# Kernel tuning notes

Measured on AMD Instinct MI355X. Metric: run time of the kernel, lower is better.

## Reference

```python
import jax, jax.numpy as jnp
import numpy as np

D = 1024          # d_model / hidden_size
F = 2048          # d_ff / intermediate_size
E = 7             # routed experts = num_experts(8) - num_shared(1)
K = 2             # top_k
AUX_COEF = 0.01


def setup_inputs() -> dict:
    key = jax.random.key(0)
    ks = jax.random.split(key, 6)
    std = 0.02
    x = jax.random.normal(ks[0], (2, 1024, D), dtype=jnp.float32)
    router_w = jax.random.normal(ks[1], (E, D), dtype=jnp.float32) * std      # Linear(D->E), no bias
    cfc_w = jax.random.normal(ks[2], (E, 2 * F, D), dtype=jnp.float32) * std  # fused gate+up per expert
    cproj_w = jax.random.normal(ks[3], (E, D, F), dtype=jnp.float32) * std    # down proj per expert
    shared_fc_w = jax.random.normal(ks[4], (2 * F, D), dtype=jnp.float32) * std
    shared_proj_w = jax.random.normal(ks[5], (D, F), dtype=jnp.float32) * std
    return {"x": x, "router_w": router_w, "cfc_w": cfc_w, "cproj_w": cproj_w,
            "shared_fc_w": shared_fc_w, "shared_proj_w": shared_proj_w}


def reference(x, router_w, cfc_w, cproj_w, shared_fc_w, shared_proj_w):
    b, s, d = x.shape
    T = b * s
    xt = x.reshape(T, d)                                     # [T, D]

    # ---- router: softmax + top-k, renormalized gates ----
    logits = xt @ router_w.T                                 # [T, E]
    probs = jax.nn.softmax(logits, axis=-1)                  # [T, E]
    topv, topi = jax.lax.top_k(probs, K)                     # [T, K]
    gates = topv / jnp.sum(topv, axis=-1, keepdims=True)     # [T, K]
    oh = jax.nn.one_hot(topi, E, dtype=probs.dtype)          # [T, K, E]
    combine = jnp.einsum('tk,tke->te', gates, oh)            # [T, E] sparse combine weights

    # ---- grouped-GEMM SwiGLU experts (dense dispatch over E) ----
    h = jnp.einsum('td,efd->tef', xt, cfc_w)                 # [T, E, 2F]
    g, u = jnp.split(h, 2, axis=-1)                          # [T, E, F] each
    act = jax.nn.silu(g) * u                                 # [T, E, F]
    act = act * combine[..., None]                           # weight before down-proj
    y = jnp.einsum('tef,edf->td', act, cproj_w)              # [T, D]

    # ---- load-balancing aux loss ----
    tokens_per_expert = jnp.mean(jnp.sum(oh, axis=1), axis=0) / K  # [E]
    mean_probs = jnp.mean(probs, axis=0)                            # [E]
    aux = (E * jnp.sum(tokens_per_expert * mean_probs)) * AUX_COEF

    # ---- shared expert (single SwiGLU, num_shared_experts == 1) ----
    hs = xt @ shared_fc_w.T                                  # [T, 2F]
    gs, us = jnp.split(hs, 2, axis=-1)
    shared = (jax.nn.silu(gs) * us) @ shared_proj_w.T        # [T, D]

    y = y + shared
    return y.reshape(b, s, d), aux.astype(x.dtype)
```

## Files before the change

### kernel.cpp

```cpp
#include <hip/hip_runtime.h>

#define TT 2048
#define DM 1024
#define FF 2048
#define NE 7
#define NSLOT 6144
#define H_LD 4096

typedef short bf16x8 __attribute__((ext_vector_type(8)));
typedef float f32x4 __attribute__((ext_vector_type(4)));

__device__ __forceinline__ unsigned short f2bf(float f) {
  union { float f; unsigned int u; } v; v.f = f;
  unsigned int r = v.u + 0x7fffu + ((v.u >> 16) & 1u);
  return (unsigned short)(r >> 16);
}
__device__ __forceinline__ float bf2f(unsigned short s) {
  union { unsigned int u; float f; } v; v.u = ((unsigned int)s) << 16;
  return v.f;
}

#define GLDS16(gp, lp)                                                        \
  __builtin_amdgcn_global_load_lds(                                           \
      (const __attribute__((address_space(1))) void*)(gp),                    \
      (__attribute__((address_space(3))) void*)(lp), 16, 0, 0)

__global__ __launch_bounds__(256) void convert_kernel(
    const float* __restrict__ src, unsigned short* __restrict__ dst) {
  size_t i = ((size_t)blockIdx.x * 256 + threadIdx.x) * 8;
  float4 a = *(const float4*)(src + i);
  float4 b = *(const float4*)(src + i + 4);
  bf16x8 o;
  o[0]=(short)f2bf(a.x); o[1]=(short)f2bf(a.y); o[2]=(short)f2bf(a.z); o[3]=(short)f2bf(a.w);
  o[4]=(short)f2bf(b.x); o[5]=(short)f2bf(b.y); o[6]=(short)f2bf(b.z); o[7]=(short)f2bf(b.w);
  *(bf16x8*)(dst + i) = o;
}

__global__ __launch_bounds__(256) void router_kernel(
    const float* __restrict__ x, const float* __restrict__ rw,
    int* __restrict__ cnt, float* __restrict__ probsum,
    int* __restrict__ idxl, float* __restrict__ gwl) {
  __shared__ float ps[NE];
  int tid = threadIdx.x;
  if (tid < NE) ps[tid] = 0.f;
  __syncthreads();
  int wave = tid >> 6, lane = tid & 63;
  int t = blockIdx.x * 4 + wave;
  float xv[16];
#pragma unroll
  for (int i = 0; i < 16; ++i) xv[i] = x[(size_t)t * DM + lane + i * 64];
  float lg[NE];
#pragma unroll
  for (int e = 0; e < NE; ++e) {
    float s = 0.f;
#pragma unroll
    for (int i = 0; i < 16; ++i) s += xv[i] * rw[e * DM + lane + i * 64];
#pragma unroll
    for (int o = 32; o > 0; o >>= 1) s += __shfl_xor(s, o);
    lg[e] = s;
  }
  float m = lg[0];
#pragma unroll
  for (int e = 1; e < NE; ++e) m = fmaxf(m, lg[e]);
  float p[NE]; float sum = 0.f;
#pragma unroll
  for (int e = 0; e < NE; ++e) { p[e] = expf(lg[e] - m); sum += p[e]; }
  float inv = 1.f / sum;
  int i1 = 0; float v1 = p[0];
#pragma unroll
  for (int e = 1; e < NE; ++e) if (p[e] > v1) { v1 = p[e]; i1 = e; }
  int i2 = -1; float v2 = -1.f;
#pragma unroll
  for (int e = 0; e < NE; ++e) if (e != i1 && p[e] > v2) { v2 = p[e]; i2 = e; }
  float g1 = v1 / (v1 + v2), g2 = v2 / (v1 + v2);
  if (lane == 0) {
#pragma unroll
    for (int e = 0; e < NE; ++e) atomicAdd(&ps[e], p[e] * inv);
    int pos = atomicAdd(&cnt[i1], 1); idxl[i1 * TT + pos] = t; gwl[i1 * TT + pos] = g1;
    pos = atomicAdd(&cnt[i2], 1);     idxl[i2 * TT + pos] = t; gwl[i2 * TT + pos] = g2;
    idxl[NE * TT + t] = t; gwl[NE * TT + t] = 1.0f;
  }
  __syncthreads();
  if (tid < NE) atomicAdd(&probsum[tid], ps[tid]);
}

__global__ void finalize_kernel(int* __restrict__ cnt, int* __restrict__ offs,
                                const float* __restrict__ probsum,
                                float* __restrict__ aux_out) {
  if (threadIdx.x == 0) {
    int o = 0;
    for (int e = 0; e < NE; ++e) { offs[e] = o; o += cnt[e]; }
    offs[NE] = o;
    cnt[NE] = TT;
    double s = 0.0;
    for (int e = 0; e < NE; ++e) s += (double)cnt[e] * (double)probsum[e];
    aux_out[0] = (float)(0.01 * 7.0 * s / (4096.0 * 2048.0));
  }
}

__global__ __launch_bounds__(256) void compact_kernel(
    const int* __restrict__ cnt, const int* __restrict__ offs,
    const int* __restrict__ idxl, const float* __restrict__ gwl,
    int* __restrict__ token_s, float* __restrict__ gate_s) {
  int j = blockIdx.x * 256 + threadIdx.x;
  int e = j >> 11, pos = j & 2047;
  if (pos < cnt[e]) {
    int s = offs[e] + pos;
    token_s[s] = idxl[j];
    gate_s[s] = gwl[j];
  }
}

template <int MODE>
__global__ __launch_bounds__(256) void moe_gemm2_kernel(
    const unsigned short* __restrict__ Abase,
    const unsigned short* __restrict__ Wb,
    unsigned short* __restrict__ ActOut, float* __restrict__ Yout,
    const int* __restrict__ cnt, const int* __restrict__ offs,
    const int* __restrict__ token_s, const float* __restrict__ gate_s) {
  constexpr int NB = (MODE == 0) ? 8 : 4;
  constexpr int BROWS = NB * 16;
  constexpr int K = (MODE == 0) ? 1024 : 2048;
  constexpr int LDA = (MODE == 0) ? 1024 : 2048;
  constexpr int WSTRIDE = (MODE == 0) ? 4096 * 1024 : 1024 * 2048;

  __shared__ unsigned short As[128 * 32];
  __shared__ unsigned short Bs[BROWS * 32];

  const int e = blockIdx.z;
  const int cnt_e = cnt[e];
  const int m0 = blockIdx.y * 128;
  if (m0 >= cnt_e) return;
  const int off_e = offs[e];
  const int nb = blockIdx.x;
  const unsigned short* Bw = Wb + (size_t)e * WSTRIDE;

  const int tid = threadIdx.x;
  const int w = tid >> 6, l = tid & 63;
  const int kq = l & 3;
  const int lsub = l >> 2;

  const unsigned short* aSrc0;
  const unsigned short* aSrc1;
  {
    int r0 = w * 32 + lsub, r1 = r0 + 16;
    int rr0 = min(m0 + r0, cnt_e - 1), rr1 = min(m0 + r1, cnt_e - 1);
    int arow0 = (MODE == 0) ? token_s[off_e + rr0] : (off_e + rr0);
    int arow1 = (MODE == 0) ? token_s[off_e + rr1] : (off_e + rr1);
    aSrc0 = Abase + (size_t)arow0 * LDA + kq * 8;
    aSrc1 = Abase + (size_t)arow1 * LDA + kq * 8;
  }
  unsigned short* aDst0 = &As[(w * 32) * 32];
  unsigned short* aDst1 = &As[(w * 32 + 16) * 32];

  const unsigned short* bSrc0;
  const unsigned short* bSrc1 = nullptr;
  unsigned short* bDst0;
  unsigned short* bDst1 = nullptr;
  if (MODE == 0) {
    int r0 = w * 32 + lsub, r1 = r0 + 16;
    int w0 = (r0 < 64) ? nb * 64 + r0 : 2048 + nb * 64 + (r0 - 64);
    int w1 = (r1 < 64) ? nb * 64 + r1 : 2048 + nb * 64 + (r1 - 64);
    bSrc0 = Bw + (size_t)w0 * K + kq * 8;
    bSrc1 = Bw + (size_t)w1 * K + kq * 8;
    bDst0 = &Bs[(w * 32) * 32];
    bDst1 = &Bs[(w * 32 + 16) * 32];
  } else {
    int r0 = w * 16 + lsub;
    bSrc0 = Bw + (size_t)(nb * 64 + r0) * K + kq * 8;
    bDst0 = &Bs[(w * 16) * 32];
  }

  f32x4 acc[2][NB];
#pragma unroll
  for (int m = 0; m < 2; ++m)
#pragma unroll
    for (int n = 0; n < NB; ++n) acc[m][n] = (f32x4){0.f, 0.f, 0.f, 0.f};

  const int lr = l & 15, lh = l >> 4;

  for (int k0 = 0; k0 < K; k0 += 32) {
    __syncthreads();
    GLDS16(aSrc0 + k0, aDst0);
    GLDS16(aSrc1 + k0, aDst1);
    GLDS16(bSrc0 + k0, bDst0);
    if (MODE == 0) GLDS16(bSrc1 + k0, bDst1);
    __syncthreads();
    bf16x8 af[2], bfv[NB];
#pragma unroll
    for (int m = 0; m < 2; ++m)
      af[m] = *(const bf16x8*)&As[(w * 32 + m * 16 + lr) * 32 + lh * 8];
#pragma unroll
    for (int n = 0; n < NB; ++n)
      bfv[n] = *(const bf16x8*)&Bs[(n * 16 + lr) * 32 + lh * 8];
#pragma unroll
    for (int m = 0; m < 2; ++m)
#pragma unroll
      for (int n = 0; n < NB; ++n)
        acc[m][n] = __builtin_amdgcn_mfma_f32_16x16x32_bf16(af[m], bfv[n], acc[m][n], 0, 0, 0);
  }

#pragma unroll
  for (int m = 0; m < 2; ++m) {
#pragma unroll
    for (int j = 0; j < 4; ++j) {
      int r = w * 32 + m * 16 + lh * 4 + j;
      int gm = m0 + r;
      if (gm < cnt_e) {
        if (MODE == 0) {
          float gate = gate_s[off_e + gm];
          size_t base = (size_t)(off_e + gm) * FF + nb * 64;
#pragma unroll
          for (int n = 0; n < 4; ++n) {
            float g = acc[m][n][j], u = acc[m][n + 4][j];
            float sg = g / (1.f + __expf(-g));
            ActOut[base + n * 16 + lr] = f2bf(sg * u * gate);
          }
        } else {
          int tok = token_s[off_e + gm];
          size_t base = (size_t)tok * DM + nb * 64;
#pragma unroll
          for (int n = 0; n < 4; ++n)
            atomicAdd(&Yout[base + n * 16 + lr], acc[m][n][j]);
        }
      }
    }
  }
}

template <int MODE>
__global__ __launch_bounds__(256) void legacy_gemm_kernel(
    const unsigned short* __restrict__ Abase,
    const float* __restrict__ Bw_routed, const float* __restrict__ Bw_shared,
    unsigned short* __restrict__ Hout, float* __restrict__ Yout,
    const int* __restrict__ cnt, const int* __restrict__ offs,
    const int* __restrict__ token_s, int N, int K, int lda) {
  __shared__ unsigned short As[128 * 32];
  __shared__ unsigned short Bs[128 * 32];
  const int e = blockIdx.z;
  const int cnt_e = cnt[e];
  const int m0 = blockIdx.y * 128;
  if (m0 >= cnt_e) return;
  const int off_e = offs[e];
  const int n0 = blockIdx.x * 128;
  const float* Bw = (e == NE) ? Bw_shared : Bw_routed + (size_t)e * N * K;
  const int tid = threadIdx.x;
  const int wave = tid >> 6, lane = tid & 63;
  const int srow = tid >> 1, kh = tid & 1;
  int rr = min(m0 + srow, cnt_e - 1);
  int slot = off_e + rr;
  int arow = (MODE == 0) ? token_s[slot] : slot;
  const unsigned short* ap = Abase + (size_t)arow * lda + kh * 16;
  const float* bp = Bw + (size_t)(n0 + srow) * K + kh * 16;
  unsigned short* adst = &As[srow * 32 + kh * 16];
  unsigned short* bdst = &Bs[srow * 32 + kh * 16];
  f32x4 acc[4][4];
#pragma unroll
  for (int m = 0; m < 4; ++m)
#pragma unroll
    for (int n = 0; n < 4; ++n) acc[m][n] = (f32x4){0.f, 0.f, 0.f, 0.f};
  const int wr = wave >> 1, wc = wave & 1;
  const int lr = lane & 15, lh = lane >> 4;
  for (int k0 = 0; k0 < K; k0 += 32) {
    __syncthreads();
    bf16x8 a0 = *(const bf16x8*)(ap + k0);
    bf16x8 a1 = *(const bf16x8*)(ap + k0 + 8);
    float4 b0 = *(const float4*)(bp + k0);
    float4 b1 = *(const float4*)(bp + k0 + 4);
    float4 b2 = *(const float4*)(bp + k0 + 8);
    float4 b3 = *(const float4*)(bp + k0 + 12);
    *(bf16x8*)adst = a0;
    *(bf16x8*)(adst + 8) = a1;
    bf16x8 w0, w1;
    w0[0]=(short)f2bf(b0.x); w0[1]=(short)f2bf(b0.y); w0[2]=(short)f2bf(b0.z); w0[3]=(short)f2bf(b0.w);
    w0[4]=(short)f2bf(b1.x); w0[5]=(short)f2bf(b1.y); w0[6]=(short)f2bf(b1.z); w0[7]=(short)f2bf(b1.w);
    w1[0]=(short)f2bf(b2.x); w1[1]=(short)f2bf(b2.y); w1[2]=(short)f2bf(b2.z); w1[3]=(short)f2bf(b2.w);
    w1[4]=(short)f2bf(b3.x); w1[5]=(short)f2bf(b3.y); w1[6]=(short)f2bf(b3.z); w1[7]=(short)f2bf(b3.w);
    *(bf16x8*)bdst = w0;
    *(bf16x8*)(bdst + 8) = w1;
    __syncthreads();
    bf16x8 af[4], bfv[4];
#pragma unroll
    for (int m = 0; m < 4; ++m)
      af[m] = *(const bf16x8*)&As[(wr * 64 + m * 16 + lr) * 32 + lh * 8];
#pragma unroll
    for (int n = 0; n < 4; ++n)
      bfv[n] = *(const bf16x8*)&Bs[(wc * 64 + n * 16 + lr) * 32 + lh * 8];
#pragma unroll
    for (int m = 0; m < 4; ++m)
#pragma unroll
      for (int n = 0; n < 4; ++n)
        acc[m][n] = __builtin_amdgcn_mfma_f32_16x16x32_bf16(af[m], bfv[n], acc[m][n], 0, 0, 0);
  }
#pragma unroll
  for (int m = 0; m < 4; ++m) {
#pragma unroll
    for (int j = 0; j < 4; ++j) {
      int r = wr * 64 + m * 16 + lh * 4 + j;
      int gm = m0 + r;
      if (gm < cnt_e) {
        if (MODE == 0) {
          size_t base = (size_t)(off_e + gm) * H_LD + n0;
#pragma unroll
          for (int n = 0; n < 4; ++n)
            Hout[base + wc * 64 + n * 16 + lr] = (unsigned short)(short)f2bf(acc[m][n][j]);
        } else {
          int tok = token_s[off_e + gm];
          size_t base = (size_t)tok * DM + n0;
#pragma unroll
          for (int n = 0; n < 4; ++n)
            atomicAdd(&Yout[base + wc * 64 + n * 16 + lr], acc[m][n][j]);
        }
      }
    }
  }
}

__global__ __launch_bounds__(256) void legacy_swiglu_kernel(
    unsigned short* __restrict__ h, const float* __restrict__ gate_s) {
  int slot = blockIdx.x;
  float gate = gate_s[slot];
  unsigned short* row = h + (size_t)slot * H_LD;
  int f0 = threadIdx.x * 8;
  bf16x8 gv = *(const bf16x8*)(row + f0);
  bf16x8 uv = *(const bf16x8*)(row + f0 + FF);
  bf16x8 o;
#pragma unroll
  for (int j = 0; j < 8; ++j) {
    float g = bf2f((unsigned short)gv[j]);
    float u = bf2f((unsigned short)uv[j]);
    float sg = g / (1.f + __expf(-g));
    o[j] = (short)f2bf(sg * u * gate);
  }
  *(bf16x8*)(row + f0) = o;
}

extern "C" void kernel_launch(void* const* d_in, const int* in_sizes, int n_in,
                              void* d_out, int out_size, void* d_ws, size_t ws_size,
                              hipStream_t stream) {
  const float* x     = (const float*)d_in[0];
  const float* rw    = (const float*)d_in[1];
  const float* cfc   = (const float*)d_in[2];
  const float* cproj = (const float*)d_in[3];
  const float* sfc   = (const float*)d_in[4];
  const float* sproj = (const float*)d_in[5];
  float* out = (float*)d_out;

  const size_t SZ_XB  = (size_t)TT * DM * 2;
  const size_t SZ_WFC = (size_t)8 * 4096 * 1024 * 2;
  const size_t SZ_WPJ = (size_t)8 * 1024 * 2048 * 2;
  const size_t SZ_ACT = (size_t)NSLOT * FF * 2;
  const size_t SZ_LISTS = (size_t)8 * TT * 8 + (size_t)NSLOT * 8 + 384;
  const size_t need_new = SZ_XB + SZ_WFC + SZ_WPJ + SZ_ACT + SZ_LISTS;

  hipMemsetAsync(d_out, 0, (size_t)out_size * sizeof(float), stream);

  if (ws_size >= need_new) {
    char* w = (char*)d_ws;
    unsigned short* xb    = (unsigned short*)w; w += SZ_XB;
    unsigned short* wfc_b = (unsigned short*)w; w += SZ_WFC;
    unsigned short* wpj_b = (unsigned short*)w; w += SZ_WPJ;
    unsigned short* act   = (unsigned short*)w; w += SZ_ACT;
    int*   idxl    = (int*)w;   w += (size_t)8 * TT * 4;
    float* gwl     = (float*)w; w += (size_t)8 * TT * 4;
    int*   token_s = (int*)w;   w += (size_t)NSLOT * 4;
    float* gate_s  = (float*)w; w += (size_t)NSLOT * 4;
    int*   cnt     = (int*)w;   w += 32;
    float* probsum = (float*)w; w += 32;
    int*   offs    = (int*)w;   w += 32;

    hipMemsetAsync(cnt, 0, 64, stream);

    convert_kernel<<<1024, 256, 0, stream>>>(x, xb);
    convert_kernel<<<14336, 256, 0, stream>>>(cfc, wfc_b);
    convert_kernel<<<2048, 256, 0, stream>>>(sfc, wfc_b + (size_t)7 * 4096 * 1024);
    convert_kernel<<<7168, 256, 0, stream>>>(cproj, wpj_b);
    convert_kernel<<<1024, 256, 0, stream>>>(sproj, wpj_b + (size_t)7 * 1024 * 2048);

    router_kernel<<<512, 256, 0, stream>>>(x, rw, cnt, probsum, idxl, gwl);
    finalize_kernel<<<1, 64, 0, stream>>>(cnt, offs, probsum, out + 2097152);
    compact_kernel<<<64, 256, 0, stream>>>(cnt, offs, idxl, gwl, token_s, gate_s);

    moe_gemm2_kernel<0><<<dim3(32, 16, 8), 256, 0, stream>>>(
        xb, wfc_b, act, nullptr, cnt, offs, token_s, gate_s);
    moe_gemm2_kernel<1><<<dim3(16, 16, 8), 256, 0, stream>>>(
        act, wpj_b, nullptr, out, cnt, offs, token_s, gate_s);
  } else {
    char* w = (char*)d_ws;
    unsigned short* xb = (unsigned short*)w; w += (size_t)TT * DM * 2;
    unsigned short* h  = (unsigned short*)w; w += (size_t)NSLOT * H_LD * 2;
    int*   idxl    = (int*)w;   w += (size_t)8 * TT * 4;
    float* gwl     = (float*)w; w += (size_t)8 * TT * 4;
    int*   token_s = (int*)w;   w += (size_t)NSLOT * 4;
    float* gate_s  = (float*)w; w += (size_t)NSLOT * 4;
    int*   cnt     = (int*)w;   w += 32;
    float* probsum = (float*)w; w += 32;
    int*   offs    = (int*)w;   w += 32;

    hipMemsetAsync(cnt, 0, 64, stream);
    convert_kernel<<<1024, 256, 0, stream>>>(x, xb);
    router_kernel<<<512, 256, 0, stream>>>(x, rw, cnt, probsum, idxl, gwl);
    finalize_kernel<<<1, 64, 0, stream>>>(cnt, offs, probsum, out + 2097152);
    compact_kernel<<<64, 256, 0, stream>>>(cnt, offs, idxl, gwl, token_s, gate_s);
    legacy_gemm_kernel<0><<<dim3(32, 16, 8), 256, 0, stream>>>(
        xb, cfc, sfc, h, nullptr, cnt, offs, token_s, 4096, 1024, 1024);
    legacy_swiglu_kernel<<<NSLOT, 256, 0, stream>>>(h, gate_s);
    legacy_gemm_kernel<1><<<dim3(8, 16, 8), 256, 0, stream>>>(
        h, cproj, sproj, nullptr, out, cnt, offs, token_s, 1024, 2048, 4096);
  }
}
```

Baseline: 466.0 us.

## Double-buffer GEMM LDS tiles and replace down-proj atomics with per-slot partials plus gather

The MoE GEMM kernels now double-buffer the A and B tiles in LDS, issuing the next k-slice's global-to-LDS loads before computing the current one, with a single barrier per iteration. The down projection no longer does fp32 atomicAdd into the output. It writes per-slot partial rows into a scratch buffer that reuses the fc-weight workspace, and a new gather kernel sums the shared-expert row and the two routed rows for each token. An inverse token-to-slot map is built in the compact kernel, and the output memset is moved to the fallback path only. This trades atomic contention for an extra partial write and read pass, and assumes every token has exactly two routed slots.

Measured after the change: 475.5 us. 2.0% more time.

```diff
diff --git a/kernel.cpp b/kernel.cpp
--- a/kernel.cpp
+++ b/kernel.cpp
@@ -98,24 +98,31 @@
   }
 }
 
+template <int INV>
 __global__ __launch_bounds__(256) void compact_kernel(
     const int* __restrict__ cnt, const int* __restrict__ offs,
     const int* __restrict__ idxl, const float* __restrict__ gwl,
-    int* __restrict__ token_s, float* __restrict__ gate_s) {
+    int* __restrict__ token_s, float* __restrict__ gate_s,
+    int* __restrict__ invn, int* __restrict__ invslot) {
   int j = blockIdx.x * 256 + threadIdx.x;
   int e = j >> 11, pos = j & 2047;
   if (pos < cnt[e]) {
     int s = offs[e] + pos;
-    token_s[s] = idxl[j];
+    int t = idxl[j];
+    token_s[s] = t;
     gate_s[s] = gwl[j];
+    if (INV && e < NE) {
+      int c = atomicAdd(&invn[t], 1);
+      invslot[t * 2 + c] = s;
+    }
   }
 }
 
 template <int MODE>
-__global__ __launch_bounds__(256) void moe_gemm2_kernel(
+__global__ __launch_bounds__(256) void moe_gemm3_kernel(
     const unsigned short* __restrict__ Abase,
     const unsigned short* __restrict__ Wb,
-    unsigned short* __restrict__ ActOut, float* __restrict__ Yout,
+    unsigned short* __restrict__ ActOut, float* __restrict__ PartOut,
     const int* __restrict__ cnt, const int* __restrict__ offs,
     const int* __restrict__ token_s, const float* __restrict__ gate_s) {
   constexpr int NB = (MODE == 0) ? 8 : 4;
@@ -124,8 +131,8 @@
   constexpr int LDA = (MODE == 0) ? 1024 : 2048;
   constexpr int WSTRIDE = (MODE == 0) ? 4096 * 1024 : 1024 * 2048;
 
-  __shared__ unsigned short As[128 * 32];
-  __shared__ unsigned short Bs[BROWS * 32];
+  __shared__ unsigned short As[2][128 * 32];
+  __shared__ unsigned short Bs[2][BROWS * 32];
 
   const int e = blockIdx.z;
   const int cnt_e = cnt[e];
@@ -150,25 +157,24 @@
     aSrc0 = Abase + (size_t)arow0 * LDA + kq * 8;
     aSrc1 = Abase + (size_t)arow1 * LDA + kq * 8;
   }
-  unsigned short* aDst0 = &As[(w * 32) * 32];
-  unsigned short* aDst1 = &As[(w * 32 + 16) * 32];
+  const int aOff0 = (w * 32) * 32;
+  const int aOff1 = (w * 32 + 16) * 32;
 
   const unsigned short* bSrc0;
   const unsigned short* bSrc1 = nullptr;
-  unsigned short* bDst0;
-  unsigned short* bDst1 = nullptr;
+  int bOff0 = 0, bOff1 = 0;
   if (MODE == 0) {
     int r0 = w * 32 + lsub, r1 = r0 + 16;
     int w0 = (r0 < 64) ? nb * 64 + r0 : 2048 + nb * 64 + (r0 - 64);
     int w1 = (r1 < 64) ? nb * 64 + r1 : 2048 + nb * 64 + (r1 - 64);
     bSrc0 = Bw + (size_t)w0 * K + kq * 8;
     bSrc1 = Bw + (size_t)w1 * K + kq * 8;
-    bDst0 = &Bs[(w * 32) * 32];
-    bDst1 = &Bs[(w * 32 + 16) * 32];
+    bOff0 = (w * 32) * 32;
+    bOff1 = (w * 32 + 16) * 32;
   } else {
     int r0 = w * 16 + lsub;
     bSrc0 = Bw + (size_t)(nb * 64 + r0) * K + kq * 8;
-    bDst0 = &Bs[(w * 16) * 32];
+    bOff0 = (w * 16) * 32;
   }
 
   f32x4 acc[2][NB];
@@ -179,25 +185,35 @@
 
   const int lr = l & 15, lh = l >> 4;
 
+  GLDS16(aSrc0, &As[0][aOff0]);
+  GLDS16(aSrc1, &As[0][aOff1]);
+  GLDS16(bSrc0, &Bs[0][bOff0]);
+  if (MODE == 0) GLDS16(bSrc1, &Bs[0][bOff1]);
+  __syncthreads();
+
+  int buf = 0;
   for (int k0 = 0; k0 < K; k0 += 32) {
-    __syncthreads();
-    GLDS16(aSrc0 + k0, aDst0);
-    GLDS16(aSrc1 + k0, aDst1);
-    GLDS16(bSrc0 + k0, bDst0);
-    if (MODE == 0) GLDS16(bSrc1 + k0, bDst1);
-    __syncthreads();
+    if (k0 + 32 < K) {
+      int nk = k0 + 32, b2 = buf ^ 1;
+      GLDS16(aSrc0 + nk, &As[b2][aOff0]);
+      GLDS16(aSrc1 + nk, &As[b2][aOff1]);
+      GLDS16(bSrc0 + nk, &Bs[b2][bOff0]);
+      if (MODE == 0) GLDS16(bSrc1 + nk, &Bs[b2][bOff1]);
+    }
     bf16x8 af[2], bfv[NB];
 #pragma unroll
     for (int m = 0; m < 2; ++m)
-      af[m] = *(const bf16x8*)&As[(w * 32 + m * 16 + lr) * 32 + lh * 8];
+      af[m] = *(const bf16x8*)&As[buf][(w * 32 + m * 16 + lr) * 32 + lh * 8];
 #pragma unroll
     for (int n = 0; n < NB; ++n)
-      bfv[n] = *(const bf16x8*)&Bs[(n * 16 + lr) * 32 + lh * 8];
+      bfv[n] = *(const bf16x8*)&Bs[buf][(n * 16 + lr) * 32 + lh * 8];
 #pragma unroll
     for (int m = 0; m < 2; ++m)
 #pragma unroll
       for (int n = 0; n < NB; ++n)
         acc[m][n] = __builtin_amdgcn_mfma_f32_16x16x32_bf16(af[m], bfv[n], acc[m][n], 0, 0, 0);
+    __syncthreads();
+    buf ^= 1;
   }
 
 #pragma unroll
@@ -217,15 +233,29 @@
             ActOut[base + n * 16 + lr] = f2bf(sg * u * gate);
           }
         } else {
-          int tok = token_s[off_e + gm];
-          size_t base = (size_t)tok * DM + nb * 64;
+          size_t base = (size_t)(off_e + gm) * DM + nb * 64;
 #pragma unroll
           for (int n = 0; n < 4; ++n)
-            atomicAdd(&Yout[base + n * 16 + lr], acc[m][n][j]);
+            PartOut[base + n * 16 + lr] = acc[m][n][j];
         }
       }
     }
   }
+}
+
+__global__ __launch_bounds__(256) void gather_kernel(
+    const float* __restrict__ part, const int* __restrict__ invslot,
+    float* __restrict__ y) {
+  int t = blockIdx.x;
+  int d = threadIdx.x * 4;
+  int s0 = invslot[t * 2], s1 = invslot[t * 2 + 1];
+  float4 a = *(const float4*)(part + (size_t)(4096 + t) * DM + d);
+  float4 b = *(const float4*)(part + (size_t)s0 * DM + d);
+  float4 c = *(const float4*)(part + (size_t)s1 * DM + d);
+  float4 o;
+  o.x = a.x + b.x + c.x; o.y = a.y + b.y + c.y;
+  o.z = a.z + b.z + c.z; o.w = a.w + b.w + c.w;
+  *(float4*)(y + (size_t)t * DM + d) = o;
 }
 
 template <int MODE>
@@ -350,10 +380,9 @@
   const size_t SZ_WFC = (size_t)8 * 4096 * 1024 * 2;
   const size_t SZ_WPJ = (size_t)8 * 1024 * 2048 * 2;
   const size_t SZ_ACT = (size_t)NSLOT * FF * 2;
-  const size_t SZ_LISTS = (size_t)8 * TT * 8 + (size_t)NSLOT * 8 + 384;
+  const size_t SZ_LISTS = (size_t)8 * TT * 8 + (size_t)NSLOT * 8
+                        + (size_t)TT * 4 + (size_t)2 * TT * 4 + 384;
   const size_t need_new = SZ_XB + SZ_WFC + SZ_WPJ + SZ_ACT + SZ_LISTS;
-
-  hipMemsetAsync(d_out, 0, (size_t)out_size * sizeof(float), stream);
 
   if (ws_size >= need_new) {
     char* w = (char*)d_ws;
@@ -365,11 +394,15 @@
     float* gwl     = (float*)w; w += (size_t)8 * TT * 4;
     int*   token_s = (int*)w;   w += (size_t)NSLOT * 4;
     float* gate_s  = (float*)w; w += (size_t)NSLOT * 4;
+    int*   invn    = (int*)w;   w += (size_t)TT * 4;
+    int*   invslot = (int*)w;   w += (size_t)2 * TT * 4;
     int*   cnt     = (int*)w;   w += 32;
     float* probsum = (float*)w; w += 32;
     int*   offs    = (int*)w;   w += 32;
+    float* part = (float*)wfc_b;
 
     hipMemsetAsync(cnt, 0, 64, stream);
+    hipMemsetAsync(invn, 0, (size_t)TT * 4, stream);
 
     convert_kernel<<<1024, 256, 0, stream>>>(x, xb);
     convert_kernel<<<14336, 256, 0, stream>>>(cfc, wfc_b);
@@ -379,12 +412,14 @@
 
     router_kernel<<<512, 256, 0, stream>>>(x, rw, cnt, probsum, idxl, gwl);
     finalize_kernel<<<1, 64, 0, stream>>>(cnt, offs, probsum, out + 2097152);
-    compact_kernel<<<64, 256, 0, stream>>>(cnt, offs, idxl, gwl, token_s, gate_s);
-
-    moe_gemm2_kernel<0><<<dim3(32, 16, 8), 256, 0, stream>>>(
+    compact_kernel<1><<<64, 256, 0, stream>>>(cnt, offs, idxl, gwl, token_s,
+                                              gate_s, invn, invslot);
+
+    moe_gemm3_kernel<0><<<dim3(32, 16, 8), 256, 0, stream>>>(
         xb, wfc_b, act, nullptr, cnt, offs, token_s, gate_s);
-    moe_gemm2_kernel<1><<<dim3(16, 16, 8), 256, 0, stream>>>(
-        act, wpj_b, nullptr, out, cnt, offs, token_s, gate_s);
+    moe_gemm3_kernel<1><<<dim3(16, 16, 8), 256, 0, stream>>>(
+        act, wpj_b, nullptr, part, cnt, offs, token_s, gate_s);
+    gather_kernel<<<TT, 256, 0, stream>>>(part, invslot, out);
   } else {
     char* w = (char*)d_ws;
     unsigned short* xb = (unsigned short*)w; w += (size_t)TT * DM * 2;
@@ -397,11 +432,13 @@
     float* probsum = (float*)w; w += 32;
     int*   offs    = (int*)w;   w += 32;
 
+    hipMemsetAsync(d_out, 0, (size_t)out_size * sizeof(float), stream);
     hipMemsetAsync(cnt, 0, 64, stream);
     convert_kernel<<<1024, 256, 0, stream>>>(x, xb);
     router_kernel<<<512, 256, 0, stream>>>(x, rw, cnt, probsum, idxl, gwl);
     finalize_kernel<<<1, 64, 0, stream>>>(cnt, offs, probsum, out + 2097152);
-    compact_kernel<<<64, 256, 0, stream>>>(cnt, offs, idxl, gwl, token_s, gate_s);
+    compact_kernel<0><<<64, 256, 0, stream>>>(cnt, offs, idxl, gwl, token_s,
+                                              gate_s, nullptr, nullptr);
     legacy_gemm_kernel<0><<<dim3(32, 16, 8), 256, 0, stream>>>(
         xb, cfc, sfc, h, nullptr, cnt, offs, token_s, 4096, 1024, 1024);
     legacy_swiglu_kernel<<<NSLOT, 256, 0, stream>>>(h, gate_s);
```
